# Performance work log

Hardware: AMD Instinct MI355X
Metric: run time of the kernel (lower is better)

The kernel has to match this reference:

```python
import jax, jax.numpy as jnp
import numpy as np

B, I, H, T = 65536, 64, 64, 16  # batch, input_size, hidden_size, type_num


def setup_inputs() -> dict:
    key = jax.random.key(0)
    ks = jax.random.split(key, 10)
    s = 0.1  # ~1/sqrt(H) init scale like torch GRUCell
    return {
        "x": jax.random.normal(ks[0], (B, I), jnp.float32),
        "typ": jax.random.randint(ks[1], (B,), 0, T, jnp.int32),
        "c": jax.random.normal(ks[2], (B, H), jnp.float32),
        "registers": jax.random.normal(ks[3], (B, T, H), jnp.float32),
        # per-type GRUCell bank (stacked across types)
        "Wih": jax.random.normal(ks[4], (T, 3 * H, I), jnp.float32) * s,
        "Whh": jax.random.normal(ks[5], (T, 3 * H, H), jnp.float32) * s,
        "bih": jax.random.normal(ks[6], (T, 3 * H), jnp.float32) * s,
        "bhh": jax.random.normal(ks[7], (T, 3 * H), jnp.float32) * s,
        # core GRUCell: input = flattened registers (T*H)
        "cWih": jax.random.normal(ks[8], (3 * H, T * H), jnp.float32) * s,
        "cWhh": jax.random.normal(ks[9], (3 * H, H), jnp.float32) * s,
        "cbih": jnp.zeros((3 * H,), jnp.float32),
        "cbhh": jnp.zeros((3 * H,), jnp.float32),
    }


def _gru(gi, gh, h):
    # torch.nn.GRUCell math; gi/gh: (..., 3H), h: (..., H)
    ir, iz, in_ = jnp.split(gi, 3, axis=-1)
    hr, hz, hn = jnp.split(gh, 3, axis=-1)
    r = jax.nn.sigmoid(ir + hr)
    z = jax.nn.sigmoid(iz + hz)
    n = jnp.tanh(in_ + r * hn)
    return (1.0 - z) * n + z * h


def reference(x, typ, c, registers, Wih, Whh, bih, bhh, cWih, cWhh, cbih, cbhh):
    # Bank of T GRUCells, all run on the same input x with per-type hidden = registers[:, t]
    gi = jnp.einsum('bi,tgi->btg', x, Wih) + bih[None]            # (B,T,3H)
    gh = jnp.einsum('bth,tgh->btg', registers, Whh) + bhh[None]   # (B,T,3H)
    hidden_tmp = _gru(gi, gh, registers)                          # (B,T,H)

    # Gather/scatter register update: only slot typ[b] takes its GRU output,
    # all other slots keep the old register (exactly what hidden_all[N, I] does).
    mask = (jnp.arange(T)[None, :] == typ[:, None])[..., None]    # (B,T,1)
    reg_new = jnp.where(mask, hidden_tmp, registers)              # (B,T,H)

    # core_v2: core GRUCell over flattened registers with state c
    xflat = reg_new.reshape(B, T * H)
    cgi = xflat @ cWih.T + cbih
    cgh = c @ cWhh.T + cbhh
    core = _gru(cgi, cgh, c)                                      # (B,H)
    return core
```

## Files before the change

kernel.cpp:

```cpp
#include <hip/hip_runtime.h>
#include <hip/hip_bf16.h>

typedef unsigned short u16;
typedef unsigned int u32;
typedef __bf16 bf16x8 __attribute__((ext_vector_type(8)));
typedef float f32x4 __attribute__((ext_vector_type(4)));


__device__ __forceinline__ u16 f2bf(float f) {
  union { float f; u32 u; } v; v.f = f;
  u32 u = v.u;
  return (u16)((u + 0x7fffu + ((u >> 16) & 1u)) >> 16);
}
__device__ __forceinline__ u32 pk2(float a, float b) {
  union { __hip_bfloat162 h; u32 u; } v;
  v.h = __float22bfloat162_rn(float2{a, b});
  return v.u;
}
__device__ __forceinline__ bf16x8 pack8(float4 a, float4 b) {
  union { u32 u[4]; bf16x8 v; } r;
  r.u[0] = pk2(a.x, a.y); r.u[1] = pk2(a.z, a.w);
  r.u[2] = pk2(b.x, b.y); r.u[3] = pk2(b.z, b.w);
  return r.v;
}
__device__ __forceinline__ float sigf(float x) { return 1.0f / (1.0f + __expf(-x)); }
__device__ __forceinline__ float tanh_fast(float x) { return 2.0f * sigf(2.0f * x) - 1.0f; }

__device__ __forceinline__ void gl_lds16(const void* g, void* l) {
  __builtin_amdgcn_global_load_lds(
      (const __attribute__((address_space(1))) unsigned int*)g,
      (__attribute__((address_space(3))) unsigned int*)l, 16, 0, 0);
}

__global__ __launch_bounds__(256) void k0_convert(
    const float* __restrict__ Wih, const float* __restrict__ Whh,
    const float* __restrict__ cWih, const float* __restrict__ cWhh,
    u16* __restrict__ wih_bf, u16* __restrict__ whh_bf,
    u16* __restrict__ cwih_bf, u16* __restrict__ cwhh_bf, int* __restrict__ gcnt)
{
  int i = blockIdx.x * 256 + threadIdx.x;
  if (blockIdx.x == 0 && threadIdx.x < 16) gcnt[threadIdx.x] = 0;
  if (i < 196608) {
    wih_bf[i]  = f2bf(Wih[i]);
    whh_bf[i]  = f2bf(Whh[i]);
    cwih_bf[i] = f2bf(cWih[i]);
  }
  if (i < 12288) cwhh_bf[i] = f2bf(cWhh[i]);
}

__global__ __launch_bounds__(256) void k_compact(
    const int* __restrict__ typ, int* __restrict__ gcnt, int* __restrict__ lists)
{
  __shared__ int cnt[16], base[16];
  const int tid = threadIdx.x;
  if (tid < 16) cnt[tid] = 0;
  __syncthreads();
  int r = blockIdx.x * 256 + tid;
  int t = typ[r];
  int rank = atomicAdd(&cnt[t], 1);
  __syncthreads();
  if (tid < 16) base[tid] = atomicAdd(&gcnt[tid], cnt[tid]);
  __syncthreads();
  lists[(size_t)t * 65536 + base[t] + rank] = r;
}

__global__ __launch_bounds__(256, 2) void k1_gru(
    const float* __restrict__ x, const float* __restrict__ regs,
    const u16* __restrict__ wih_bf, const u16* __restrict__ whh_bf,
    const float* __restrict__ bih, const float* __restrict__ bhh,
    const int* __restrict__ gcnt, const int* __restrict__ lists,
    float* __restrict__ modslot)
{
  const int t = blockIdx.y;
  const int cnt = gcnt[t];
  const int ntiles = (cnt + 15) >> 4;

  const int tid = threadIdx.x;
  const int lane = tid & 63;
  const int w = tid >> 6;
  const int col = lane & 15;
  const int quad = lane >> 4;
  const int hidx = w * 16 + col;
  const f32x4 zero = {0.f, 0.f, 0.f, 0.f};

  bf16x8 bw[3][2], bh[3][2];
  float vbi[3], vbh[3];
#pragma unroll
  for (int g = 0; g < 3; ++g) {
    const u16* pw = wih_bf + ((size_t)t * 192 + g * 64 + hidx) * 64;
    const u16* ph = whh_bf + ((size_t)t * 192 + g * 64 + hidx) * 64;
#pragma unroll
    for (int ks = 0; ks < 2; ++ks) {
      bw[g][ks] = *(const bf16x8*)(pw + ks * 32 + quad * 8);
      bh[g][ks] = *(const bf16x8*)(ph + ks * 32 + quad * 8);
    }
    vbi[g] = bih[t * 192 + g * 64 + hidx];
    vbh[g] = bhh[t * 192 + g * 64 + hidx];
  }

  __shared__ int s_rows[16];

  for (int tile = blockIdx.x; tile < ntiles; tile += 32) {
    __syncthreads();
    if (tid < 16) {
      int idx = tile * 16 + tid;
      s_rows[tid] = lists[(size_t)t * 65536 + (idx < cnt ? idx : cnt - 1)];
    }
    __syncthreads();

    const int ra = s_rows[col];
    f32x4 agi[3], agh[3];
#pragma unroll
    for (int g = 0; g < 3; ++g) { agi[g] = zero; agh[g] = zero; }
#pragma unroll
    for (int ks = 0; ks < 2; ++ks) {
      const float* xr = x + (size_t)ra * 64 + ks * 32 + quad * 8;
      const float* hr = regs + (size_t)ra * 1024 + t * 64 + ks * 32 + quad * 8;
      bf16x8 ax = pack8(*(const float4*)xr, *(const float4*)(xr + 4));
      bf16x8 ah = pack8(*(const float4*)hr, *(const float4*)(hr + 4));
#pragma unroll
      for (int g = 0; g < 3; ++g) {
        agi[g] = __builtin_amdgcn_mfma_f32_16x16x32_bf16(ax, bw[g][ks], agi[g], 0, 0, 0);
        agh[g] = __builtin_amdgcn_mfma_f32_16x16x32_bf16(ah, bh[g][ks], agh[g], 0, 0, 0);
      }
    }
#pragma unroll
    for (int rr = 0; rr < 4; ++rr) {
      int m = quad * 4 + rr;
      if (tile * 16 + m < cnt) {
        int r2 = s_rows[m];
        float ir  = agi[0][rr] + vbi[0];
        float iz  = agi[1][rr] + vbi[1];
        float in_ = agi[2][rr] + vbi[2];
        float hr  = agh[0][rr] + vbh[0];
        float hz  = agh[1][rr] + vbh[1];
        float hn  = agh[2][rr] + vbh[2];
        float rg = sigf(ir + hr);
        float zg = sigf(iz + hz);
        float ng = tanh_fast(in_ + rg * hn);
        float hold = regs[(size_t)r2 * 1024 + t * 64 + hidx];
        float hnew = (1.f - zg) * ng + zg * hold;
        modslot[(size_t)r2 * 64 + hidx] = hnew;
      }
    }
  }
}

__global__ __launch_bounds__(256, 2) void k2_core(
    const float* __restrict__ regs, const float* __restrict__ c,
    const int* __restrict__ typ, const float* __restrict__ modslot,
    const u16* __restrict__ cwih_bf, const u16* __restrict__ cwhh_bf,
    const float* __restrict__ cbih, const float* __restrict__ cbhh,
    float* __restrict__ out)
{
  __shared__ __align__(16) float sA[2][4096];
  __shared__ __align__(16) u16  sB[2][12288];

  const int tid = threadIdx.x;
  const int b0 = blockIdx.x * 64;
  const int lane = tid & 63;
  const int wv = tid >> 6;
  const int col = lane & 15;
  const int quad = lane >> 4;
  const int hidx = wv * 16 + col;
  const f32x4 zero = {0.f, 0.f, 0.f, 0.f};

  const int grp = lane & 15;
  const float* pA[4];
  const float* pM[4];
  int t4[4];
#pragma unroll
  for (int s = 0; s < 4; ++s) {
    int i = s * 4 + wv;
    int r = i * 4 + (lane >> 4);
    int swz = (grp ^ (r & 15)) << 2;
    pA[s] = regs + (size_t)(b0 + r) * 1024 + swz;
    pM[s] = modslot + (size_t)(b0 + r) * 64 + swz;
    t4[s] = typ[b0 + r];
  }

  {
#pragma unroll
    for (int s = 0; s < 4; ++s) {
      const float* src = (t4[s] == 0) ? pM[s] : pA[s];
      gl_lds16(src, &sA[0][(s * 4 + wv) * 256]);
    }
#pragma unroll
    for (int s = 0; s < 6; ++s) {
      int j = s * 4 + wv;
      int n = j * 8 + (lane >> 3);
      int grpb = lane & 7;
      gl_lds16(cwih_bf + (size_t)n * 1024 + ((grpb ^ (n & 7)) << 3), &sB[0][j * 512]);
    }
  }

  f32x4 agh[4][3];
#pragma unroll
  for (int mt = 0; mt < 4; ++mt)
#pragma unroll
    for (int g = 0; g < 3; ++g) agh[mt][g] = zero;
#pragma unroll
  for (int ks = 0; ks < 2; ++ks) {
    bf16x8 bh2[3];
#pragma unroll
    for (int g = 0; g < 3; ++g)
      bh2[g] = *(const bf16x8*)(cwhh_bf + (size_t)(g * 64 + hidx) * 64 + ks * 32 + quad * 8);
#pragma unroll
    for (int mt = 0; mt < 4; ++mt) {
      const float* cr = c + (size_t)(b0 + mt * 16 + col) * 64 + ks * 32 + quad * 8;
      bf16x8 af = pack8(*(const float4*)cr, *(const float4*)(cr + 4));
#pragma unroll
      for (int g = 0; g < 3; ++g)
        agh[mt][g] = __builtin_amdgcn_mfma_f32_16x16x32_bf16(af, bh2[g], agh[mt][g], 0, 0, 0);
    }
  }

  f32x4 agi[4][3];
#pragma unroll
  for (int mt = 0; mt < 4; ++mt)
#pragma unroll
    for (int g = 0; g < 3; ++g) agi[mt][g] = zero;

  for (int kc = 0; kc < 16; ++kc) {
    __syncthreads();
    if (kc < 15) {
      float* sAn = sA[(kc + 1) & 1];
      u16*   sBn = sB[(kc + 1) & 1];
#pragma unroll
      for (int s = 0; s < 4; ++s) {
        const float* src = (t4[s] == kc + 1) ? pM[s] : (pA[s] + (kc + 1) * 64);
        gl_lds16(src, sAn + (s * 4 + wv) * 256);
      }
#pragma unroll
      for (int s = 0; s < 6; ++s) {
        int j = s * 4 + wv;
        int n = j * 8 + (lane >> 3);
        int grpb = lane & 7;
        gl_lds16(cwih_bf + (size_t)n * 1024 + (kc + 1) * 64 + ((grpb ^ (n & 7)) << 3),
                 sBn + j * 512);
      }
    }
    const float* sAc = sA[kc & 1];
    const u16*   sBc = sB[kc & 1];
#pragma unroll
    for (int ks = 0; ks < 2; ++ks) {
      bf16x8 bfr[3];
#pragma unroll
      for (int g = 0; g < 3; ++g) {
        int n = g * 64 + hidx;
        int grpb = ks * 4 + quad;
        bfr[g] = *(const bf16x8*)(sBc + n * 64 + ((grpb ^ (n & 7)) << 3));
      }
#pragma unroll
      for (int mt = 0; mt < 4; ++mt) {
        int r = mt * 16 + col;
        int g0 = ks * 8 + quad * 2;
        float4 q0 = *(const float4*)(sAc + r * 64 + (((g0    ) ^ (r & 15)) << 2));
        float4 q1 = *(const float4*)(sAc + r * 64 + (((g0 + 1) ^ (r & 15)) << 2));
        bf16x8 af = pack8(q0, q1);
#pragma unroll
        for (int g = 0; g < 3; ++g)
          agi[mt][g] = __builtin_amdgcn_mfma_f32_16x16x32_bf16(af, bfr[g], agi[mt][g], 0, 0, 0);
      }
    }
  }

  float e0 = cbih[hidx], e1 = cbih[64 + hidx], e2 = cbih[128 + hidx];
  float d0 = cbhh[hidx], d1 = cbhh[64 + hidx], d2 = cbhh[128 + hidx];
#pragma unroll
  for (int mt = 0; mt < 4; ++mt) {
#pragma unroll
    for (int rr = 0; rr < 4; ++rr) {
      int row = mt * 16 + quad * 4 + rr;
      size_t b = (size_t)(b0 + row);
      float ir  = agi[mt][0][rr] + e0;
      float iz  = agi[mt][1][rr] + e1;
      float in_ = agi[mt][2][rr] + e2;
      float hr  = agh[mt][0][rr] + d0;
      float hz  = agh[mt][1][rr] + d1;
      float hn  = agh[mt][2][rr] + d2;
      float rg = sigf(ir + hr);
      float zg = sigf(iz + hz);
      float ng = tanh_fast(in_ + rg * hn);
      float cold = c[b * 64 + hidx];
      out[b * 64 + hidx] = (1.f - zg) * ng + zg * cold;
    }
  }
}

extern "C" void kernel_launch(void* const* d_in, const int* in_sizes, int n_in,
                              void* d_out, int out_size, void* d_ws, size_t ws_size,
                              hipStream_t stream) {
  const float* x    = (const float*)d_in[0];
  const int*   typ  = (const int*)d_in[1];
  const float* c    = (const float*)d_in[2];
  const float* regs = (const float*)d_in[3];
  const float* Wih  = (const float*)d_in[4];
  const float* Whh  = (const float*)d_in[5];
  const float* bih  = (const float*)d_in[6];
  const float* bhh  = (const float*)d_in[7];
  const float* cWih = (const float*)d_in[8];
  const float* cWhh = (const float*)d_in[9];
  const float* cbih = (const float*)d_in[10];
  const float* cbhh = (const float*)d_in[11];
  float* out = (float*)d_out;

  char* ws = (char*)d_ws;
  u16* wih_bf  = (u16*)(ws + 0);
  u16* whh_bf  = (u16*)(ws + 393216);
  u16* cwih_bf = (u16*)(ws + 786432);
  u16* cwhh_bf = (u16*)(ws + 1179648);
  int* gcnt    = (int*)(ws + 1204224);
  int* lists   = (int*)(ws + 1204288);
  float* modslot = (float*)(ws + 5398592);

  k0_convert<<<768, 256, 0, stream>>>(Wih, Whh, cWih, cWhh,
                                      wih_bf, whh_bf, cwih_bf, cwhh_bf, gcnt);
  k_compact<<<256, 256, 0, stream>>>(typ, gcnt, lists);
  k1_gru<<<dim3(32, 16), 256, 0, stream>>>(x, regs, wih_bf, whh_bf, bih, bhh,
                                           gcnt, lists, modslot);
  k2_core<<<1024, 256, 0, stream>>>(regs, c, typ, modslot, cwih_bf, cwhh_bf,
                                    cbih, cbhh, out);
}
```

Measured before the change: 467.8 us.

## Load core weights directly to registers, drop LDS B tile, raise occupancy

In k2_core, the shared-memory double buffer for the bf16 cWih tile is removed and each wave loads its B fragments straight from global memory (likely L2-resident) into registers every k-chunk. This cuts LDS to about 32KB so launch bounds can rise to 3 blocks per CU. The hidden-state GEMM for c is moved after the main loop and done per m-tile to shorten accumulator live ranges. In k1_gru, the shared row-index staging and its two barriers per tile are replaced by direct per-lane list loads, and the grid is doubled to 64 blocks per type. The risk is that the global B loads add latency and redundant L2 traffic that the higher occupancy may not hide.

```diff
diff --git a/kernel.cpp b/kernel.cpp
--- a/kernel.cpp
+++ b/kernel.cpp
@@ -98,17 +98,11 @@
     vbh[g] = bhh[t * 192 + g * 64 + hidx];
   }
 
-  __shared__ int s_rows[16];
-
-  for (int tile = blockIdx.x; tile < ntiles; tile += 32) {
-    __syncthreads();
-    if (tid < 16) {
-      int idx = tile * 16 + tid;
-      s_rows[tid] = lists[(size_t)t * 65536 + (idx < cnt ? idx : cnt - 1)];
-    }
-    __syncthreads();
-
-    const int ra = s_rows[col];
+  const int* lst = lists + (size_t)t * 65536;
+
+  for (int tile = blockIdx.x; tile < ntiles; tile += 64) {
+    const int ia = tile * 16 + col;
+    const int ra = lst[ia < cnt ? ia : cnt - 1];
     f32x4 agi[3], agh[3];
 #pragma unroll
     for (int g = 0; g < 3; ++g) { agi[g] = zero; agh[g] = zero; }
@@ -127,8 +121,9 @@
 #pragma unroll
     for (int rr = 0; rr < 4; ++rr) {
       int m = quad * 4 + rr;
-      if (tile * 16 + m < cnt) {
-        int r2 = s_rows[m];
+      int idx = tile * 16 + m;
+      if (idx < cnt) {
+        int r2 = lst[idx];
         float ir  = agi[0][rr] + vbi[0];
         float iz  = agi[1][rr] + vbi[1];
         float in_ = agi[2][rr] + vbi[2];
@@ -146,7 +141,7 @@
   }
 }
 
-__global__ __launch_bounds__(256, 2) void k2_core(
+__global__ __launch_bounds__(256, 3) void k2_core(
     const float* __restrict__ regs, const float* __restrict__ c,
     const int* __restrict__ typ, const float* __restrict__ modslot,
     const u16* __restrict__ cwih_bf, const u16* __restrict__ cwhh_bf,
@@ -154,7 +149,6 @@
     float* __restrict__ out)
 {
   __shared__ __align__(16) float sA[2][4096];
-  __shared__ __align__(16) u16  sB[2][12288];
 
   const int tid = threadIdx.x;
   const int b0 = blockIdx.x * 64;
@@ -179,78 +173,39 @@
     t4[s] = typ[b0 + r];
   }
 
-  {
-#pragma unroll
-    for (int s = 0; s < 4; ++s) {
-      const float* src = (t4[s] == 0) ? pM[s] : pA[s];
-      gl_lds16(src, &sA[0][(s * 4 + wv) * 256]);
-    }
-#pragma unroll
-    for (int s = 0; s < 6; ++s) {
-      int j = s * 4 + wv;
-      int n = j * 8 + (lane >> 3);
-      int grpb = lane & 7;
-      gl_lds16(cwih_bf + (size_t)n * 1024 + ((grpb ^ (n & 7)) << 3), &sB[0][j * 512]);
-    }
-  }
-
-  f32x4 agh[4][3];
+#pragma unroll
+  for (int s = 0; s < 4; ++s) {
+    const float* src = (t4[s] == 0) ? pM[s] : pA[s];
+    gl_lds16(src, &sA[0][(s * 4 + wv) * 256]);
+  }
+
+  f32x4 agi[4][3];
 #pragma unroll
   for (int mt = 0; mt < 4; ++mt)
 #pragma unroll
-    for (int g = 0; g < 3; ++g) agh[mt][g] = zero;
-#pragma unroll
-  for (int ks = 0; ks < 2; ++ks) {
-    bf16x8 bh2[3];
-#pragma unroll
-    for (int g = 0; g < 3; ++g)
-      bh2[g] = *(const bf16x8*)(cwhh_bf + (size_t)(g * 64 + hidx) * 64 + ks * 32 + quad * 8);
-#pragma unroll
-    for (int mt = 0; mt < 4; ++mt) {
-      const float* cr = c + (size_t)(b0 + mt * 16 + col) * 64 + ks * 32 + quad * 8;
-      bf16x8 af = pack8(*(const float4*)cr, *(const float4*)(cr + 4));
+    for (int g = 0; g < 3; ++g) agi[mt][g] = zero;
+
+  for (int kc = 0; kc < 16; ++kc) {
+    bf16x8 bfr[2][3];
+#pragma unroll
+    for (int ks = 0; ks < 2; ++ks)
 #pragma unroll
       for (int g = 0; g < 3; ++g)
-        agh[mt][g] = __builtin_amdgcn_mfma_f32_16x16x32_bf16(af, bh2[g], agh[mt][g], 0, 0, 0);
-    }
-  }
-
-  f32x4 agi[4][3];
-#pragma unroll
-  for (int mt = 0; mt < 4; ++mt)
-#pragma unroll
-    for (int g = 0; g < 3; ++g) agi[mt][g] = zero;
-
-  for (int kc = 0; kc < 16; ++kc) {
+        bfr[ks][g] = *(const bf16x8*)(cwih_bf + (size_t)(g * 64 + hidx) * 1024 + kc * 64 + ks * 32 + quad * 8);
+    __builtin_amdgcn_sched_barrier(0);
     __syncthreads();
     if (kc < 15) {
       float* sAn = sA[(kc + 1) & 1];
-      u16*   sBn = sB[(kc + 1) & 1];
 #pragma unroll
       for (int s = 0; s < 4; ++s) {
         const float* src = (t4[s] == kc + 1) ? pM[s] : (pA[s] + (kc + 1) * 64);
         gl_lds16(src, sAn + (s * 4 + wv) * 256);
       }
-#pragma unroll
-      for (int s = 0; s < 6; ++s) {
-        int j = s * 4 + wv;
-        int n = j * 8 + (lane >> 3);
-        int grpb = lane & 7;
-        gl_lds16(cwih_bf + (size_t)n * 1024 + (kc + 1) * 64 + ((grpb ^ (n & 7)) << 3),
-                 sBn + j * 512);
-      }
-    }
+    }
+    __builtin_amdgcn_sched_barrier(0);
     const float* sAc = sA[kc & 1];
-    const u16*   sBc = sB[kc & 1];
-#pragma unroll
-    for (int ks = 0; ks < 2; ++ks) {
-      bf16x8 bfr[3];
-#pragma unroll
-      for (int g = 0; g < 3; ++g) {
-        int n = g * 64 + hidx;
-        int grpb = ks * 4 + quad;
-        bfr[g] = *(const bf16x8*)(sBc + n * 64 + ((grpb ^ (n & 7)) << 3));
-      }
+#pragma unroll
+    for (int ks = 0; ks < 2; ++ks) {
 #pragma unroll
       for (int mt = 0; mt < 4; ++mt) {
         int r = mt * 16 + col;
@@ -260,15 +215,30 @@
         bf16x8 af = pack8(q0, q1);
 #pragma unroll
         for (int g = 0; g < 3; ++g)
-          agi[mt][g] = __builtin_amdgcn_mfma_f32_16x16x32_bf16(af, bfr[g], agi[mt][g], 0, 0, 0);
-      }
-    }
-  }
-
-  float e0 = cbih[hidx], e1 = cbih[64 + hidx], e2 = cbih[128 + hidx];
-  float d0 = cbhh[hidx], d1 = cbhh[64 + hidx], d2 = cbhh[128 + hidx];
+          agi[mt][g] = __builtin_amdgcn_mfma_f32_16x16x32_bf16(af, bfr[ks][g], agi[mt][g], 0, 0, 0);
+      }
+    }
+  }
+
+  const float e0 = cbih[hidx], e1 = cbih[64 + hidx], e2 = cbih[128 + hidx];
+  const float d0 = cbhh[hidx], d1 = cbhh[64 + hidx], d2 = cbhh[128 + hidx];
 #pragma unroll
   for (int mt = 0; mt < 4; ++mt) {
+    f32x4 agh[3];
+#pragma unroll
+    for (int g = 0; g < 3; ++g) agh[g] = zero;
+#pragma unroll
+    for (int ks = 0; ks < 2; ++ks) {
+      bf16x8 bh2[3];
+#pragma unroll
+      for (int g = 0; g < 3; ++g)
+        bh2[g] = *(const bf16x8*)(cwhh_bf + (size_t)(g * 64 + hidx) * 64 + ks * 32 + quad * 8);
+      const float* cr = c + (size_t)(b0 + mt * 16 + col) * 64 + ks * 32 + quad * 8;
+      bf16x8 af = pack8(*(const float4*)cr, *(const float4*)(cr + 4));
+#pragma unroll
+      for (int g = 0; g < 3; ++g)
+        agh[g] = __builtin_amdgcn_mfma_f32_16x16x32_bf16(af, bh2[g], agh[g], 0, 0, 0);
+    }
 #pragma unroll
     for (int rr = 0; rr < 4; ++rr) {
       int row = mt * 16 + quad * 4 + rr;
@@ -276,9 +246,9 @@
       float ir  = agi[mt][0][rr] + e0;
       float iz  = agi[mt][1][rr] + e1;
       float in_ = agi[mt][2][rr] + e2;
-      float hr  = agh[mt][0][rr] + d0;
-      float hz  = agh[mt][1][rr] + d1;
-      float hn  = agh[mt][2][rr] + d2;
+      float hr  = agh[0][rr] + d0;
+      float hz  = agh[1][rr] + d1;
+      float hn  = agh[2][rr] + d2;
       float rg = sigf(ir + hr);
       float zg = sigf(iz + hz);
       float ng = tanh_fast(in_ + rg * hn);
@@ -317,7 +287,7 @@
   k0_convert<<<768, 256, 0, stream>>>(Wih, Whh, cWih, cWhh,
                                       wih_bf, whh_bf, cwih_bf, cwhh_bf, gcnt);
   k_compact<<<256, 256, 0, stream>>>(typ, gcnt, lists);
-  k1_gru<<<dim3(32, 16), 256, 0, stream>>>(x, regs, wih_bf, whh_bf, bih, bhh,
+  k1_gru<<<dim3(64, 16), 256, 0, stream>>>(x, regs, wih_bf, whh_bf, bih, bhh,
                                            gcnt, lists, modslot);
   k2_core<<<1024, 256, 0, stream>>>(regs, c, typ, modslot, cwih_bf, cwhh_bf,
                                     cbih, cbhh, out);
```

Measured after the change: 478.5 us. +2.3%, slower.
